# Optimization experiments

Hardware: AMD Instinct MI355X
Metric: run time of the kernel (lower is better)

## Reference

```python
import jax, jax.numpy as jnp
import numpy as np
from jax import lax

NUM_LAYERS = 3
NUM_QUBITS = 8
BATCH = 131072
DIM = 2 ** NUM_QUBITS  # 256


def _rot_mats(params):
    # params: (L, Q, 3) angles for RX, RY, RZ. Returns combined U = RZ @ RY @ RX, (L, Q, 2, 2) complex64.
    half = params * 0.5
    cx = jnp.cos(half[..., 0]).astype(jnp.complex64)
    sx = jnp.sin(half[..., 0]).astype(jnp.complex64)
    cy = jnp.cos(half[..., 1]).astype(jnp.complex64)
    sy = jnp.sin(half[..., 1]).astype(jnp.complex64)
    ezm = jnp.exp(-1j * half[..., 2]).astype(jnp.complex64)
    ezp = jnp.exp(1j * half[..., 2]).astype(jnp.complex64)
    zero = jnp.zeros_like(cx)
    RX = jnp.stack([jnp.stack([cx, -1j * sx], -1), jnp.stack([-1j * sx, cx], -1)], -2)
    RY = jnp.stack([jnp.stack([cy, -sy], -1), jnp.stack([sy, cy], -1)], -2)
    RZ = jnp.stack([jnp.stack([ezm, zero], -1), jnp.stack([zero, ezp], -1)], -2)
    return jnp.einsum('lqij,lqjk,lqkm->lqim', RZ, RY, RX)


def _apply_1q(state, U, wire):
    # state: (B, 2,2,...,2); wire w lives on axis w+1 (PennyLane wire 0 = most significant bit)
    ax = wire + 1
    return jnp.moveaxis(jnp.tensordot(U, state, axes=((1,), (ax,))), 0, ax)


def _apply_cnot(state, ctrl, tgt):
    c_ax, t_ax = ctrl + 1, tgt + 1
    s0 = lax.index_in_dim(state, 0, axis=c_ax, keepdims=True)
    s1 = lax.index_in_dim(state, 1, axis=c_ax, keepdims=True)
    s1 = jnp.flip(s1, axis=t_ax)
    return jnp.concatenate([s0, s1], axis=c_ax)


def _circuit(params, state_re, state_im):
    U = _rot_mats(params)  # (L, Q, 2, 2)
    state = (state_re + 1j * state_im).astype(jnp.complex64)
    state = state.reshape((state.shape[0],) + (2,) * NUM_QUBITS)
    for l in range(NUM_LAYERS):
        for q in range(NUM_QUBITS):
            state = _apply_1q(state, U[l, q], q)
        for q in range(NUM_QUBITS):
            state = _apply_cnot(state, q, (q + 1) % NUM_QUBITS)
    state = state.reshape(state.shape[0], DIM)
    # probability that wire 0 measures |0>: sum |amp|^2 over first half of amplitudes
    half = state[:, : DIM // 2]
    return jnp.sum(half.real ** 2 + half.imag ** 2, axis=1).astype(jnp.float32)


def setup_inputs() -> dict:
    key = jax.random.key(0)
    k1, k2, k3 = jax.random.split(key, 3)
    params = jax.random.uniform(k1, (NUM_LAYERS, NUM_QUBITS, 3), dtype=jnp.float32)
    sr = jax.random.normal(k2, (BATCH, DIM), dtype=jnp.float32)
    si = jax.random.normal(k3, (BATCH, DIM), dtype=jnp.float32)
    norm = jnp.sqrt(jnp.sum(sr ** 2 + si ** 2, axis=1, keepdims=True))
    return {"params": params, "state_re": sr / norm, "state_im": si / norm}


def reference(params, state_re, state_im):
    return _circuit(params, state_re, state_im)
```

## Files before the change

### kernel.cpp

```cpp
#include <hip/hip_runtime.h>
#include <stdint.h>

#define NLAYERS 3
#define NQ 8
#define DIM 256
#define KDIM 512
#define BM 64
#define NBLK (131072 / BM)

typedef float  f32x4  __attribute__((ext_vector_type(4)));
typedef __bf16 bf16x8 __attribute__((ext_vector_type(8)));

__device__ __forceinline__ unsigned short f2bf(float f){
    union { float f; uint32_t u; } v; v.f = f;
    uint32_t u = v.u;
    u += 0x7fffu + ((u >> 16) & 1u);
    return (unsigned short)(u >> 16);
}

__device__ __forceinline__ float2 cmul(float2 a, float2 b){
    return make_float2(a.x*b.x - a.y*b.y, a.x*b.y + a.y*b.x);
}

__device__ __forceinline__ void gload_lds16(void* lds, const void* g){
    __builtin_amdgcn_global_load_lds(
        (const __attribute__((address_space(1))) unsigned int*)g,
        (__attribute__((address_space(3))) unsigned int*)lds,
        16, 0, 0);
}

__global__ __launch_bounds__(256) void build_g_kernel(const float* __restrict__ params,
                                                      unsigned short* __restrict__ G){
    __shared__ float2 st[2][DIM];
    __shared__ float2 gm[NLAYERS*NQ][4];
    const int j = blockIdx.x;
    const int i = threadIdx.x;

    if (i < NLAYERS*NQ){
        const float* pp = params + i*3;
        float hx = 0.5f*pp[0], hy = 0.5f*pp[1], hz = 0.5f*pp[2];
        float cx = cosf(hx), sx = sinf(hx);
        float cy = cosf(hy), sy = sinf(hy);
        float cz = cosf(hz), sz = sinf(hz);
        float2 ezm = make_float2(cz, -sz), ezp = make_float2(cz, sz);
        float2 m00 = make_float2( cy*cx,  sy*sx);
        float2 m01 = make_float2(-sy*cx, -cy*sx);
        float2 m10 = make_float2( sy*cx, -cy*sx);
        float2 m11 = make_float2( cy*cx, -sy*sx);
        gm[i][0] = cmul(ezm, m00);
        gm[i][1] = cmul(ezm, m01);
        gm[i][2] = cmul(ezp, m10);
        gm[i][3] = cmul(ezp, m11);
    }

    int psrc = i;
    #pragma unroll
    for (int q = NQ-1; q >= 0; --q){
        int c  = 7 - q;
        int tb = 7 - ((q + 1) & 7);
        psrc = ((psrc >> c) & 1) ? (psrc ^ (1 << tb)) : psrc;
    }

    int cur = 0;
    st[0][i] = make_float2(i == j ? 1.0f : 0.0f, 0.0f);
    __syncthreads();

    for (int l = 0; l < NLAYERS; ++l){
        for (int q = 0; q < NQ; ++q){
            float2 U0a = gm[l*NQ+q][0], U0b = gm[l*NQ+q][1];
            float2 U1a = gm[l*NQ+q][2], U1b = gm[l*NQ+q][3];
            int p  = 7 - q;
            int bs = (i >> p) & 1;
            int i0 = i & ~(1 << p), i1 = i | (1 << p);
            float2 a0 = st[cur][i0], a1 = st[cur][i1];
            float2 ua = bs ? U1a : U0a;
            float2 ub = bs ? U1b : U0b;
            float2 r;
            r.x = ua.x*a0.x - ua.y*a0.y + ub.x*a1.x - ub.y*a1.y;
            r.y = ua.x*a0.y + ua.y*a0.x + ub.x*a1.y + ub.y*a1.x;
            st[cur ^ 1][i] = r;
            cur ^= 1;
            __syncthreads();
        }
        float2 r = st[cur][psrc];
        st[cur ^ 1][i] = r;
        cur ^= 1;
        __syncthreads();
    }

    const int m = i & 127;
    float2 a = st[cur][m];
    unsigned short lo, hi;
    if (i < 128){ lo = f2bf(a.x); hi = f2bf(-a.y); }
    else        { lo = f2bf(a.y); hi = f2bf( a.x); }
    G[(size_t)i*KDIM + j]        = lo;
    G[(size_t)i*KDIM + j + DIM]  = hi;
}

__global__ __launch_bounds__(256, 3) void qform_kernel(const float* __restrict__ sr,
                                                       const float* __restrict__ si,
                                                       const unsigned short* __restrict__ G,
                                                       float* __restrict__ out){
    __shared__ float          As[BM * 64];
    __shared__ unsigned short Bs[DIM * 64];
    __shared__ float red[4 * BM];

    const int tid  = threadIdx.x;
    const int lane = tid & 63;
    const int w    = tid >> 6;
    const int l15  = lane & 15;
    const int quad = lane >> 4;
    const int x7   = l15 & 7;
    const size_t mbase = (size_t)blockIdx.x * BM;

    f32x4 acc[4][4];
    const f32x4 vzero = {0.0f, 0.0f, 0.0f, 0.0f};
    #pragma unroll
    for (int ii = 0; ii < 4; ++ii)
        #pragma unroll
        for (int jj = 0; jj < 4; ++jj)
            acc[ii][jj] = vzero;

    for (int kc = 0; kc < 8; ++kc){
        __syncthreads();
        {
            const float* Zsrc = (kc < 4) ? sr : si;
            const int kcol = (kc & 3) * 64;
            #pragma unroll
            for (int i = 0; i < 4; ++i){
                const int c  = w*4 + i;
                const int ar = c*4 + (lane >> 4);
                const int gg = (lane & 15) ^ (ar & 7);
                const float* gp = Zsrc + (mbase + ar)*DIM + kcol + gg*4;
                gload_lds16(&As[c*256], gp);
            }
        }
        {
            #pragma unroll
            for (int i = 0; i < 8; ++i){
                const int c  = w*8 + i;
                const int rb = c*8 + (lane >> 3);
                const int gb = (lane & 7) ^ (rb & 7);
                const unsigned short* gp = G + (size_t)rb*KDIM + kc*64 + gb*8;
                gload_lds16(&Bs[c*512], gp);
            }
        }
        __syncthreads();

        #pragma unroll
        for (int ks = 0; ks < 2; ++ks){
            bf16x8 a[4], b[4];
            const int g0 = ks*8 + quad*2;
            #pragma unroll
            for (int ii = 0; ii < 4; ++ii){
                const int m = ii*16 + l15;
                union { float4 v; uint32_t u[4]; } h0, h1;
                h0.v = *(const float4*)&As[m*64 + ((g0    ) ^ x7)*4];
                h1.v = *(const float4*)&As[m*64 + ((g0 + 1) ^ x7)*4];
                union { uint32_t u[4]; bf16x8 f; } pk;
                pk.u[0] = __builtin_amdgcn_perm(h0.u[1], h0.u[0], 0x07060302);
                pk.u[1] = __builtin_amdgcn_perm(h0.u[3], h0.u[2], 0x07060302);
                pk.u[2] = __builtin_amdgcn_perm(h1.u[1], h1.u[0], 0x07060302);
                pk.u[3] = __builtin_amdgcn_perm(h1.u[3], h1.u[2], 0x07060302);
                a[ii] = pk.f;
            }
            const int gB = ks*4 + quad;
            #pragma unroll
            for (int jj = 0; jj < 4; ++jj){
                const int n = w*64 + jj*16 + l15;
                b[jj] = *(const bf16x8*)&Bs[n*64 + (gB ^ x7)*8];
            }
            #pragma unroll
            for (int ii = 0; ii < 4; ++ii)
                #pragma unroll
                for (int jj = 0; jj < 4; ++jj)
                    acc[ii][jj] = __builtin_amdgcn_mfma_f32_16x16x32_bf16(
                        a[ii], b[jj], acc[ii][jj], 0, 0, 0);
        }
    }

    float s[4][4];
    #pragma unroll
    for (int ii = 0; ii < 4; ++ii)
        #pragma unroll
        for (int r = 0; r < 4; ++r){
            float t = 0.0f;
            #pragma unroll
            for (int jj = 0; jj < 4; ++jj){ float v = acc[ii][jj][r]; t += v*v; }
            s[ii][r] = t;
        }
    #pragma unroll
    for (int ii = 0; ii < 4; ++ii)
        #pragma unroll
        for (int r = 0; r < 4; ++r){
            float t = s[ii][r];
            t += __shfl_xor(t, 1);
            t += __shfl_xor(t, 2);
            t += __shfl_xor(t, 4);
            t += __shfl_xor(t, 8);
            s[ii][r] = t;
        }
    if (l15 == 0){
        #pragma unroll
        for (int ii = 0; ii < 4; ++ii)
            #pragma unroll
            for (int r = 0; r < 4; ++r)
                red[w*64 + ii*16 + quad*4 + r] = s[ii][r];
    }
    __syncthreads();
    if (tid < 64){
        float o = red[tid] + red[64 + tid] + red[128 + tid] + red[192 + tid];
        out[mbase + tid] = o;
    }
}

extern "C" void kernel_launch(void* const* d_in, const int* in_sizes, int n_in,
                              void* d_out, int out_size, void* d_ws, size_t ws_size,
                              hipStream_t stream){
    const float* params = (const float*)d_in[0];
    const float* sr     = (const float*)d_in[1];
    const float* si     = (const float*)d_in[2];
    unsigned short* G   = (unsigned short*)d_ws;
    float* out          = (float*)d_out;

    build_g_kernel<<<dim3(DIM), dim3(256), 0, stream>>>(params, G);
    qform_kernel<<<dim3(NBLK), dim3(256), 0, stream>>>(sr, si, G, out);
}
```

Before: 289.3 us.

## Convert full A tile to bf16 in LDS upfront and read G directly from global

The A tile (64 rows × 512 complex components) is now loaded once with plain vector loads, rounded to bf16 and stored in a padded LDS buffer, replacing the eight-stage chunked global_load_lds loop with per-chunk barriers. B fragments are read straight from global (L2-resident G) instead of being staged in LDS, and the K loop runs 16 MFMA steps with no intermediate syncs. The aim is to remove repeated barriers and LDS staging for B. The cost is no overlap between the A load and compute, global-latency-bound B fragment loads inside the MFMA loop, and lower declared occupancy (2 blocks per CU instead of 3).

Result: slower. 336.3 us (+16.2%).

```diff
diff --git a/kernel.cpp b/kernel.cpp
--- a/kernel.cpp
+++ b/kernel.cpp
@@ -6,6 +6,7 @@
 #define DIM 256
 #define KDIM 512
 #define BM 64
+#define AST 520
 #define NBLK (131072 / BM)
 
 typedef float  f32x4  __attribute__((ext_vector_type(4)));
@@ -20,13 +21,6 @@
 
 __device__ __forceinline__ float2 cmul(float2 a, float2 b){
     return make_float2(a.x*b.x - a.y*b.y, a.x*b.y + a.y*b.x);
-}
-
-__device__ __forceinline__ void gload_lds16(void* lds, const void* g){
-    __builtin_amdgcn_global_load_lds(
-        (const __attribute__((address_space(1))) unsigned int*)g,
-        (__attribute__((address_space(3))) unsigned int*)lds,
-        16, 0, 0);
 }
 
 __global__ __launch_bounds__(256) void build_g_kernel(const float* __restrict__ params,
@@ -97,12 +91,11 @@
     G[(size_t)i*KDIM + j + DIM]  = hi;
 }
 
-__global__ __launch_bounds__(256, 3) void qform_kernel(const float* __restrict__ sr,
+__global__ __launch_bounds__(256, 2) void qform_kernel(const float* __restrict__ sr,
                                                        const float* __restrict__ si,
                                                        const unsigned short* __restrict__ G,
                                                        float* __restrict__ out){
-    __shared__ float          As[BM * 64];
-    __shared__ unsigned short Bs[DIM * 64];
+    __shared__ unsigned short As[BM * AST];
     __shared__ float red[4 * BM];
 
     const int tid  = threadIdx.x;
@@ -110,8 +103,28 @@
     const int w    = tid >> 6;
     const int l15  = lane & 15;
     const int quad = lane >> 4;
-    const int x7   = l15 & 7;
     const size_t mbase = (size_t)blockIdx.x * BM;
+
+    {
+        const int r  = tid >> 2;
+        const int cs = (tid & 3) * 64;
+        #pragma unroll
+        for (int h = 0; h < 2; ++h){
+            const float* gp = (h ? si : sr) + (mbase + r)*DIM + cs;
+            unsigned short* dst = &As[r*AST + h*256 + cs];
+            #pragma unroll
+            for (int o = 0; o < 8; ++o){
+                float4 fa = ((const float4*)gp)[o*2];
+                float4 fb = ((const float4*)gp)[o*2+1];
+                uint4 pk;
+                pk.x = f2bf(fa.x) | ((uint32_t)f2bf(fa.y) << 16);
+                pk.y = f2bf(fa.z) | ((uint32_t)f2bf(fa.w) << 16);
+                pk.z = f2bf(fb.x) | ((uint32_t)f2bf(fb.y) << 16);
+                pk.w = f2bf(fb.z) | ((uint32_t)f2bf(fb.w) << 16);
+                *(uint4*)(dst + o*8) = pk;
+            }
+        }
+    }
 
     f32x4 acc[4][4];
     const f32x4 vzero = {0.0f, 0.0f, 0.0f, 0.0f};
@@ -121,62 +134,25 @@
         for (int jj = 0; jj < 4; ++jj)
             acc[ii][jj] = vzero;
 
-    for (int kc = 0; kc < 8; ++kc){
-        __syncthreads();
-        {
-            const float* Zsrc = (kc < 4) ? sr : si;
-            const int kcol = (kc & 3) * 64;
-            #pragma unroll
-            for (int i = 0; i < 4; ++i){
-                const int c  = w*4 + i;
-                const int ar = c*4 + (lane >> 4);
-                const int gg = (lane & 15) ^ (ar & 7);
-                const float* gp = Zsrc + (mbase + ar)*DIM + kcol + gg*4;
-                gload_lds16(&As[c*256], gp);
-            }
-        }
-        {
-            #pragma unroll
-            for (int i = 0; i < 8; ++i){
-                const int c  = w*8 + i;
-                const int rb = c*8 + (lane >> 3);
-                const int gb = (lane & 7) ^ (rb & 7);
-                const unsigned short* gp = G + (size_t)rb*KDIM + kc*64 + gb*8;
-                gload_lds16(&Bs[c*512], gp);
-            }
-        }
-        __syncthreads();
-
-        #pragma unroll
-        for (int ks = 0; ks < 2; ++ks){
-            bf16x8 a[4], b[4];
-            const int g0 = ks*8 + quad*2;
-            #pragma unroll
-            for (int ii = 0; ii < 4; ++ii){
-                const int m = ii*16 + l15;
-                union { float4 v; uint32_t u[4]; } h0, h1;
-                h0.v = *(const float4*)&As[m*64 + ((g0    ) ^ x7)*4];
-                h1.v = *(const float4*)&As[m*64 + ((g0 + 1) ^ x7)*4];
-                union { uint32_t u[4]; bf16x8 f; } pk;
-                pk.u[0] = __builtin_amdgcn_perm(h0.u[1], h0.u[0], 0x07060302);
-                pk.u[1] = __builtin_amdgcn_perm(h0.u[3], h0.u[2], 0x07060302);
-                pk.u[2] = __builtin_amdgcn_perm(h1.u[1], h1.u[0], 0x07060302);
-                pk.u[3] = __builtin_amdgcn_perm(h1.u[3], h1.u[2], 0x07060302);
-                a[ii] = pk.f;
-            }
-            const int gB = ks*4 + quad;
-            #pragma unroll
-            for (int jj = 0; jj < 4; ++jj){
-                const int n = w*64 + jj*16 + l15;
-                b[jj] = *(const bf16x8*)&Bs[n*64 + (gB ^ x7)*8];
-            }
-            #pragma unroll
-            for (int ii = 0; ii < 4; ++ii)
-                #pragma unroll
-                for (int jj = 0; jj < 4; ++jj)
-                    acc[ii][jj] = __builtin_amdgcn_mfma_f32_16x16x32_bf16(
-                        a[ii], b[jj], acc[ii][jj], 0, 0, 0);
-        }
+    const unsigned short* gB = G + ((size_t)(w*64 + l15))*KDIM + quad*8;
+
+    __syncthreads();
+
+    #pragma unroll 4
+    for (int ks = 0; ks < 16; ++ks){
+        bf16x8 a[4], b[4];
+        #pragma unroll
+        for (int jj = 0; jj < 4; ++jj)
+            b[jj] = *(const bf16x8*)(gB + (size_t)jj*16*KDIM + ks*32);
+        #pragma unroll
+        for (int ii = 0; ii < 4; ++ii)
+            a[ii] = *(const bf16x8*)&As[(ii*16 + l15)*AST + ks*32 + quad*8];
+        #pragma unroll
+        for (int ii = 0; ii < 4; ++ii)
+            #pragma unroll
+            for (int jj = 0; jj < 4; ++jj)
+                acc[ii][jj] = __builtin_amdgcn_mfma_f32_16x16x32_bf16(
+                    a[ii], b[jj], acc[ii][jj], 0, 0, 0);
     }
 
     float s[4][4];
```
